# Kernel optimization log

Measured on AMD Instinct MI355X. Metric: run time of the kernel, lower is better.

Reference implementation:

```python
import jax, jax.numpy as jnp
import numpy as np

B, S, D, O = 1, 2048, 512, 512
H, QD, K, PK = 8, 256, 16, 256
N = PK * PK  # 65536 experts
HALF = QD // 2  # sub-query dim per product-key dimension


def _l2norm(x):
    # matches F.normalize(dim=-1): x / max(||x||, 1e-12)
    n = jnp.sqrt(jnp.sum(x * x, axis=-1, keepdims=True))
    return x / jnp.maximum(n, 1e-12)


def setup_inputs() -> dict:
    key = jax.random.key(0)
    ks = jax.random.split(key, 9)
    return {
        "hidden_states": jax.random.normal(ks[0], (B, S, D), jnp.float32),
        "Wq": jax.random.normal(ks[1], (H * QD, D), jnp.float32) * 0.02,
        "bq": jnp.zeros((H * QD,), jnp.float32),
        "ln_g": jnp.ones((QD,), jnp.float32),
        "ln_b": jnp.zeros((QD,), jnp.float32),
        "keys0": jax.random.normal(ks[2], (PK, HALF), jnp.float32) * 0.02,
        "keys1": jax.random.normal(ks[3], (PK, HALF), jnp.float32) * 0.02,
        "expert_down": jax.random.normal(ks[4], (N, D), jnp.float32) * 0.02,
        "expert_up": jax.random.normal(ks[5], (N, O), jnp.float32) * 0.02,
    }


def reference(hidden_states, Wq, bq, ln_g, ln_b, keys0, keys1, expert_down, expert_up):
    b, s, d = hidden_states.shape
    # query projection + layernorm over query_dim
    q = (hidden_states @ Wq.T + bq).reshape(b, s, H, QD)
    mu = jnp.mean(q, axis=-1, keepdims=True)
    var = jnp.mean((q - mu) ** 2, axis=-1, keepdims=True)
    q = (q - mu) / jnp.sqrt(var + 1e-5) * ln_g + ln_b
    # split into per-dimension sub-queries, normalize queries and keys
    q0, q1 = q[..., :HALF], q[..., HALF:]
    s0 = jnp.einsum('bshq,eq->bshe', _l2norm(q0), _l2norm(keys0))  # [b,s,H,PK]
    s1 = jnp.einsum('bshq,eq->bshe', _l2norm(q1), _l2norm(keys1))
    # per-dim top-k' (k' = K=16 here due to clamping logic in source)
    sc0, ix0 = jax.lax.top_k(s0, K)
    sc1, ix1 = jax.lax.top_k(s1, K)
    # combinatorial merge: scores add; NOTE source adds indices with multiplier 1
    # for the last dim and never scales the first-dim indices (faithful repro).
    cs = (sc0[..., :, None] + sc1[..., None, :]).reshape(b, s, H, K * K)
    ci = (ix0[..., :, None] + ix1[..., None, :]).reshape(b, s, H, K * K)
    fs, pos = jax.lax.top_k(cs, K)
    fi = jnp.take_along_axis(ci, pos, axis=-1)  # [b,s,H,K] expert ids
    w = jax.nn.softmax(fs, axis=-1)
    # gather rank-1 experts and apply: down-project, gelu, up-project, combine
    down = expert_down[fi]  # [b,s,H,K,D]
    up = expert_up[fi]      # [b,s,H,K,O]
    inner = jnp.einsum('bsd,bshkd->bshk', hidden_states, down)
    act = jax.nn.gelu(inner, approximate=False)
    out = jnp.einsum('bshk,bshko->bso', act * w, up)
    return out
```

## Files before the change

### kernel.cpp

```cpp
#include <hip/hip_runtime.h>
#include <math.h>

constexpr int Sx    = 2048;
constexpr int Dx    = 512;
constexpr int Hx    = 8;
constexpr int QDx   = 256;
constexpr int HALFx = 128;
constexpr int PKx   = 256;
constexpr int Kx    = 16;
constexpr int HQx   = Hx * QDx;
constexpr int Rx    = Sx * Hx;
constexpr int Ox    = 512;

__global__ __launch_bounds__(64) void knorm_kernel(
    const float* __restrict__ k0, const float* __restrict__ k1,
    float* __restrict__ k0n, float* __restrict__ k1n)
{
    const int row = blockIdx.x;
    const float* src = (row < PKx) ? (k0 + (size_t)row * HALFx)
                                   : (k1 + (size_t)(row - PKx) * HALFx);
    float* dst = (row < PKx) ? (k0n + (size_t)row * HALFx)
                             : (k1n + (size_t)(row - PKx) * HALFx);
    const int t = threadIdx.x;
    float a = src[t];
    float b = src[t + 64];
    float ss = a * a + b * b;
#pragma unroll
    for (int off = 32; off; off >>= 1) ss += __shfl_xor(ss, off);
    float n = sqrtf(ss);
    n = fmaxf(n, 1e-12f);
    dst[t]      = a / n;
    dst[t + 64] = b / n;
}

__global__ __launch_bounds__(256) void qproj_kernel(
    const float* __restrict__ A,
    const float* __restrict__ W,
    const float* __restrict__ bq,
    float* __restrict__ C)
{
    constexpr int BM = 64, BN = 64, BK = 32, PAD = 4;
    __shared__ __align__(16) float As[BK][BM + PAD];
    __shared__ __align__(16) float Bs[BK][BN + PAD];
    const int bm = blockIdx.y * BM;
    const int bn = blockIdx.x * BN;
    const int tid = threadIdx.x;
    const int tx = tid & 15;
    const int ty = tid >> 4;
    float acc[4][4] = {{0.f}};
    for (int k0 = 0; k0 < Dx; k0 += BK) {
#pragma unroll
        for (int i = 0; i < (BM * BK) / 256; ++i) {
            int idx = tid + i * 256;
            int m = idx >> 5;
            int k = idx & 31;
            As[k][m] = A[(size_t)(bm + m) * Dx + k0 + k];
            Bs[k][m] = W[(size_t)(bn + m) * Dx + k0 + k];
        }
        __syncthreads();
#pragma unroll
        for (int k = 0; k < BK; ++k) {
            float4 av = *(const float4*)&As[k][ty * 4];
            float4 bv = *(const float4*)&Bs[k][tx * 4];
            float a4[4] = {av.x, av.y, av.z, av.w};
            float b4[4] = {bv.x, bv.y, bv.z, bv.w};
#pragma unroll
            for (int i = 0; i < 4; ++i)
#pragma unroll
                for (int j = 0; j < 4; ++j)
                    acc[i][j] = fmaf(a4[i], b4[j], acc[i][j]);
        }
        __syncthreads();
    }
#pragma unroll
    for (int i = 0; i < 4; ++i) {
        const int row = bm + ty * 4 + i;
#pragma unroll
        for (int j = 0; j < 4; ++j) {
            const int col = bn + tx * 4 + j;
            C[(size_t)row * HQx + col] = acc[i][j] + bq[col];
        }
    }
}

__global__ __launch_bounds__(64) void ln_kernel(
    float* __restrict__ q, const float* __restrict__ g,
    const float* __restrict__ b)
{
    const int r = blockIdx.x;
    float* row = q + (size_t)r * QDx;
    const int t = threadIdx.x;
    float v0 = row[t], v1 = row[t + 64], v2 = row[t + 128], v3 = row[t + 192];
    float sum = v0 + v1 + v2 + v3;
#pragma unroll
    for (int off = 32; off; off >>= 1) sum += __shfl_xor(sum, off);
    const float mu = sum * (1.f / 256.f);
    float d0 = v0 - mu, d1 = v1 - mu, d2 = v2 - mu, d3 = v3 - mu;
    float ss = d0 * d0 + d1 * d1 + d2 * d2 + d3 * d3;
#pragma unroll
    for (int off = 32; off; off >>= 1) ss += __shfl_xor(ss, off);
    const float var = ss * (1.f / 256.f);
    const float inv = 1.0f / sqrtf(var + 1e-5f);
    v0 = d0 * inv * g[t]       + b[t];
    v1 = d1 * inv * g[t + 64]  + b[t + 64];
    v2 = d2 * inv * g[t + 128] + b[t + 128];
    v3 = d3 * inv * g[t + 192] + b[t + 192];
    float s0 = v0 * v0 + v1 * v1;
#pragma unroll
    for (int off = 32; off; off >>= 1) s0 += __shfl_xor(s0, off);
    float n0 = fmaxf(sqrtf(s0), 1e-12f);
    float s1 = v2 * v2 + v3 * v3;
#pragma unroll
    for (int off = 32; off; off >>= 1) s1 += __shfl_xor(s1, off);
    float n1 = fmaxf(sqrtf(s1), 1e-12f);
    row[t]       = v0 / n0;
    row[t + 64]  = v1 / n0;
    row[t + 128] = v2 / n1;
    row[t + 192] = v3 / n1;
}

__global__ __launch_bounds__(256) void score_kernel(
    const float* __restrict__ qn,
    const float* __restrict__ k0n, const float* __restrict__ k1n,
    float* __restrict__ s0, float* __restrict__ s1)
{
    constexpr int BM = 64, BN = 64, BK = 32, PAD = 4;
    __shared__ __align__(16) float As[BK][BM + PAD];
    __shared__ __align__(16) float Bs[BK][BN + PAD];
    const int half = blockIdx.z;
    const float* B = half ? k1n : k0n;
    float* Sout = half ? s1 : s0;
    const int bm = blockIdx.y * BM;
    const int bn = blockIdx.x * BN;
    const int tid = threadIdx.x;
    const int tx = tid & 15;
    const int ty = tid >> 4;
    const int coff = half * HALFx;
    float acc[4][4] = {{0.f}};
    for (int k0 = 0; k0 < HALFx; k0 += BK) {
#pragma unroll
        for (int i = 0; i < (BM * BK) / 256; ++i) {
            int idx = tid + i * 256;
            int m = idx >> 5;
            int k = idx & 31;
            As[k][m] = qn[(size_t)(bm + m) * QDx + coff + k0 + k];
            Bs[k][m] = B[(size_t)(bn + m) * HALFx + k0 + k];
        }
        __syncthreads();
#pragma unroll
        for (int k = 0; k < BK; ++k) {
            float4 av = *(const float4*)&As[k][ty * 4];
            float4 bv = *(const float4*)&Bs[k][tx * 4];
            float a4[4] = {av.x, av.y, av.z, av.w};
            float b4[4] = {bv.x, bv.y, bv.z, bv.w};
#pragma unroll
            for (int i = 0; i < 4; ++i)
#pragma unroll
                for (int j = 0; j < 4; ++j)
                    acc[i][j] = fmaf(a4[i], b4[j], acc[i][j]);
        }
        __syncthreads();
    }
#pragma unroll
    for (int i = 0; i < 4; ++i)
#pragma unroll
        for (int j = 0; j < 4; ++j)
            Sout[(size_t)(bm + ty * 4 + i) * PKx + bn + tx * 4 + j] = acc[i][j];
}

__device__ inline void wave_top16(float v[4], int lane, float* outv, int* outi)
{
#pragma unroll 1
    for (int it = 0; it < 16; ++it) {
        float m = v[0];
        int mi = lane;
#pragma unroll
        for (int j = 1; j < 4; ++j) {
            int idx = lane + 64 * j;
            if (v[j] > m) { m = v[j]; mi = idx; }
        }
#pragma unroll
        for (int off = 32; off; off >>= 1) {
            float om = __shfl_xor(m, off);
            int oi = __shfl_xor(mi, off);
            if (om > m || (om == m && oi < mi)) { m = om; mi = oi; }
        }
        if (lane == 0) { outv[it] = m; outi[it] = mi; }
        if ((mi & 63) == lane) v[mi >> 6] = -INFINITY;
    }
}

__global__ __launch_bounds__(64) void topk_kernel(
    const float* __restrict__ s0g, const float* __restrict__ s1g,
    int* __restrict__ fib, float* __restrict__ wb)
{
    __shared__ float sc0[Kx], sc1[Kx], fsv[Kx];
    __shared__ int ix0[Kx], ix1[Kx], fpos[Kx];
    const int r = blockIdx.x;
    const int lane = threadIdx.x;
    float v[4];
#pragma unroll
    for (int j = 0; j < 4; ++j) v[j] = s0g[(size_t)r * PKx + lane + 64 * j];
    wave_top16(v, lane, sc0, ix0);
#pragma unroll
    for (int j = 0; j < 4; ++j) v[j] = s1g[(size_t)r * PKx + lane + 64 * j];
    wave_top16(v, lane, sc1, ix1);
    __syncthreads();
#pragma unroll
    for (int j = 0; j < 4; ++j) {
        int p = lane + 64 * j;
        v[j] = sc0[p >> 4] + sc1[p & 15];
    }
    wave_top16(v, lane, fsv, fpos);
    __syncthreads();
    float f = fsv[lane & 15];
    float mx = f;
#pragma unroll
    for (int off = 8; off; off >>= 1) mx = fmaxf(mx, __shfl_xor(mx, off, 16));
    float e = expf(f - mx);
    float sum = e;
#pragma unroll
    for (int off = 8; off; off >>= 1) sum += __shfl_xor(sum, off, 16);
    if (lane < Kx) {
        int p = fpos[lane];
        fib[(size_t)r * Kx + lane] = ix0[p >> 4] + ix1[p & 15];
        wb[(size_t)r * Kx + lane]  = e / sum;
    }
}

__global__ __launch_bounds__(256) void expert_kernel(
    const float* __restrict__ hidden, const float* __restrict__ down,
    const float* __restrict__ up, const int* __restrict__ fib,
    const float* __restrict__ wb, float* __restrict__ out)
{
    __shared__ float hs[Dx];
    __shared__ float aw[Hx * Kx];
    __shared__ int fis[Hx * Kx];
    const int s = blockIdx.x;
    const int tid = threadIdx.x;
    hs[tid]       = hidden[(size_t)s * Dx + tid];
    hs[tid + 256] = hidden[(size_t)s * Dx + tid + 256];
    if (tid < Hx * Kx) fis[tid] = fib[(size_t)s * (Hx * Kx) + tid];
    __syncthreads();
    const int wv = tid >> 6;
    const int lane = tid & 63;
    for (int p = wv; p < Hx * Kx; p += 4) {
        const float* dr = down + (size_t)fis[p] * Dx;
        float acc = 0.f;
#pragma unroll
        for (int i = 0; i < 8; ++i)
            acc = fmaf(hs[lane + 64 * i], dr[lane + 64 * i], acc);
#pragma unroll
        for (int off = 32; off; off >>= 1) acc += __shfl_xor(acc, off);
        if (lane == 0) {
            float x = acc;
            float act = 0.5f * x * (1.f + erff(x * 0.70710678118654752f));
            aw[p] = act * wb[(size_t)s * (Hx * Kx) + p];
        }
    }
    __syncthreads();
    float a0 = 0.f, a1 = 0.f;
    for (int p = 0; p < Hx * Kx; ++p) {
        const float a = aw[p];
        const float* ur = up + (size_t)fis[p] * Ox;
        a0 = fmaf(a, ur[tid], a0);
        a1 = fmaf(a, ur[tid + 256], a1);
    }
    out[(size_t)s * Ox + tid]       = a0;
    out[(size_t)s * Ox + tid + 256] = a1;
}

extern "C" void kernel_launch(void* const* d_in, const int* in_sizes, int n_in,
                              void* d_out, int out_size, void* d_ws, size_t ws_size,
                              hipStream_t stream)
{
    const float* hidden = (const float*)d_in[0];
    const float* Wq     = (const float*)d_in[1];
    const float* bq     = (const float*)d_in[2];
    const float* ln_g   = (const float*)d_in[3];
    const float* ln_b   = (const float*)d_in[4];
    const float* keys0  = (const float*)d_in[5];
    const float* keys1  = (const float*)d_in[6];
    const float* edown  = (const float*)d_in[7];
    const float* eup    = (const float*)d_in[8];
    float* out = (float*)d_out;

    float* ws  = (float*)d_ws;
    float* q   = ws;
    float* k0n = q + (size_t)Sx * HQx;
    float* k1n = k0n + (size_t)PKx * HALFx;
    float* s0  = k1n + (size_t)PKx * HALFx;
    float* s1  = s0 + (size_t)Rx * PKx;
    float* wb  = s1 + (size_t)Rx * PKx;
    int*   fib = (int*)(wb + (size_t)Rx * Kx);

    hipLaunchKernelGGL(knorm_kernel, dim3(2 * PKx), dim3(64), 0, stream,
                       keys0, keys1, k0n, k1n);
    hipLaunchKernelGGL(qproj_kernel, dim3(HQx / 64, Sx / 64), dim3(256), 0, stream,
                       hidden, Wq, bq, q);
    hipLaunchKernelGGL(ln_kernel, dim3(Rx), dim3(64), 0, stream, q, ln_g, ln_b);
    hipLaunchKernelGGL(score_kernel, dim3(PKx / 64, Rx / 64, 2), dim3(256), 0, stream,
                       q, k0n, k1n, s0, s1);
    hipLaunchKernelGGL(topk_kernel, dim3(Rx), dim3(64), 0, stream, s0, s1, fib, wb);
    hipLaunchKernelGGL(expert_kernel, dim3(Sx), dim3(256), 0, stream,
                       hidden, edown, eup, fib, wb, out);
}
```

Baseline: 491.8 us.

## Replace iterative wave argmax top-16 with radix-select threshold and ballot compaction

The top-k kernel used to pull out 16 maxima one at a time with wave shuffle reductions. It now finds the 16th-largest value by a 32-step bitwise radix search over order-preserving integer keys, counting candidates with ballot and popcount. It then compacts the selected elements with prefix popcounts, and merges the combined indices inline. This removes the serial shuffle reductions, but the output comes out in unsorted order and ties may be ordered differently from the reference.

```diff
diff --git a/kernel.cpp b/kernel.cpp
--- a/kernel.cpp
+++ b/kernel.cpp
@@ -168,25 +168,36 @@
             Sout[(size_t)(bm + ty * 4 + i) * PKx + bn + tx * 4 + j] = acc[i][j];
 }
 
-__device__ inline void wave_top16(float v[4], int lane, float* outv, int* outi)
-{
-#pragma unroll 1
-    for (int it = 0; it < 16; ++it) {
-        float m = v[0];
-        int mi = lane;
-#pragma unroll
-        for (int j = 1; j < 4; ++j) {
-            int idx = lane + 64 * j;
-            if (v[j] > m) { m = v[j]; mi = idx; }
-        }
-#pragma unroll
-        for (int off = 32; off; off >>= 1) {
-            float om = __shfl_xor(m, off);
-            int oi = __shfl_xor(mi, off);
-            if (om > m || (om == m && oi < mi)) { m = om; mi = oi; }
-        }
-        if (lane == 0) { outv[it] = m; outi[it] = mi; }
-        if ((mi & 63) == lane) v[mi >> 6] = -INFINITY;
+__device__ __forceinline__ unsigned fkey(float f) {
+    unsigned u = __float_as_uint(f);
+    return u ^ ((u & 0x80000000u) ? 0xFFFFFFFFu : 0x80000000u);
+}
+
+__device__ __forceinline__ void extract16(
+    const float v[4], const unsigned u[4], unsigned T, int lane,
+    unsigned long long lmask, float* outv, int* outi)
+{
+    unsigned long long mg[4];
+    int gt_total = 0;
+#pragma unroll
+    for (int j = 0; j < 4; ++j) {
+        mg[j] = __ballot(u[j] > T);
+        gt_total += __popcll(mg[j]);
+    }
+    int bg = 0, be = gt_total;
+#pragma unroll
+    for (int j = 0; j < 4; ++j) {
+        unsigned long long me = __ballot(u[j] == T);
+        int idx = lane + 64 * j;
+        if (u[j] > T) {
+            int pg = bg + __popcll(mg[j] & lmask);
+            outv[pg] = v[j]; outi[pg] = idx;
+        } else if (u[j] == T) {
+            int pe = be + __popcll(me & lmask);
+            if (pe < 16) { outv[pe] = v[j]; outi[pe] = idx; }
+        }
+        bg += __popcll(mg[j]);
+        be += __popcll(me);
     }
 }
 
@@ -195,24 +206,81 @@
     int* __restrict__ fib, float* __restrict__ wb)
 {
     __shared__ float sc0[Kx], sc1[Kx], fsv[Kx];
-    __shared__ int ix0[Kx], ix1[Kx], fpos[Kx];
+    __shared__ int ix0[Kx], ix1[Kx], fid[Kx];
     const int r = blockIdx.x;
     const int lane = threadIdx.x;
-    float v[4];
-#pragma unroll
-    for (int j = 0; j < 4; ++j) v[j] = s0g[(size_t)r * PKx + lane + 64 * j];
-    wave_top16(v, lane, sc0, ix0);
-#pragma unroll
-    for (int j = 0; j < 4; ++j) v[j] = s1g[(size_t)r * PKx + lane + 64 * j];
-    wave_top16(v, lane, sc1, ix1);
+    const unsigned long long lmask = (1ull << lane) - 1ull;
+
+    float v0[4], v1[4];
+    unsigned u0[4], u1[4];
+#pragma unroll
+    for (int j = 0; j < 4; ++j) {
+        v0[j] = s0g[(size_t)r * PKx + lane + 64 * j];
+        v1[j] = s1g[(size_t)r * PKx + lane + 64 * j];
+        u0[j] = fkey(v0[j]);
+        u1[j] = fkey(v1[j]);
+    }
+
+    unsigned T0 = 0, T1 = 0;
+    for (int bit = 31; bit >= 0; --bit) {
+        const unsigned c0 = T0 | (1u << bit);
+        const unsigned c1 = T1 | (1u << bit);
+        int n0 = 0, n1 = 0;
+#pragma unroll
+        for (int j = 0; j < 4; ++j) {
+            n0 += __popcll(__ballot(u0[j] >= c0));
+            n1 += __popcll(__ballot(u1[j] >= c1));
+        }
+        if (n0 >= Kx) T0 = c0;
+        if (n1 >= Kx) T1 = c1;
+    }
+    extract16(v0, u0, T0, lane, lmask, sc0, ix0);
+    extract16(v1, u1, T1, lane, lmask, sc1, ix1);
     __syncthreads();
+
+    float cv[4];
+    unsigned cu[4];
+    int ci[4];
 #pragma unroll
     for (int j = 0; j < 4; ++j) {
         int p = lane + 64 * j;
-        v[j] = sc0[p >> 4] + sc1[p & 15];
-    }
-    wave_top16(v, lane, fsv, fpos);
+        cv[j] = sc0[p >> 4] + sc1[p & 15];
+        cu[j] = fkey(cv[j]);
+        ci[j] = ix0[p >> 4] + ix1[p & 15];
+    }
+    unsigned T2 = 0;
+    for (int bit = 31; bit >= 0; --bit) {
+        const unsigned c2 = T2 | (1u << bit);
+        int n2 = 0;
+#pragma unroll
+        for (int j = 0; j < 4; ++j) n2 += __popcll(__ballot(cu[j] >= c2));
+        if (n2 >= Kx) T2 = c2;
+    }
+    {
+        unsigned long long mg[4];
+        int gt_total = 0;
+#pragma unroll
+        for (int j = 0; j < 4; ++j) {
+            mg[j] = __ballot(cu[j] > T2);
+            gt_total += __popcll(mg[j]);
+        }
+        int bg = 0, be = gt_total;
+#pragma unroll
+        for (int j = 0; j < 4; ++j) {
+            unsigned long long me = __ballot(cu[j] == T2);
+            if (cu[j] > T2) {
+                int pg = bg + __popcll(mg[j] & lmask);
+                fsv[pg] = cv[j]; fid[pg] = ci[j];
+            } else if (cu[j] == T2) {
+                int pe = be + __popcll(me & lmask);
+                if (pe < 16) { fsv[pe] = cv[j]; fid[pe] = ci[j]; }
+            }
+            bg += __popcll(mg[j]);
+            be += __popcll(me);
+        }
+    }
     __syncthreads();
+
     float f = fsv[lane & 15];
     float mx = f;
 #pragma unroll
@@ -222,8 +290,7 @@
 #pragma unroll
     for (int off = 8; off; off >>= 1) sum += __shfl_xor(sum, off, 16);
     if (lane < Kx) {
-        int p = fpos[lane];
-        fib[(size_t)r * Kx + lane] = ix0[p >> 4] + ix1[p & 15];
+        fib[(size_t)r * Kx + lane] = fid[lane];
         wb[(size_t)r * Kx + lane]  = e / sum;
     }
 }
```

Result: faster. 407.2 us (-17.2%).
